# Kernel optimization log

Hardware: AMD Instinct MI355X
Metric: run time of the kernel (lower is better)

Reference implementation:

```python
import jax, jax.numpy as jnp
import numpy as np
import math

MODEL_DIM = 256
NUM_HEADS = 8
HEAD_DIM = MODEL_DIM // NUM_HEADS
DEMAND_DIM = 3
H, W = 128, 256
N_COLLAB = 4


def conv1x1(x, w, b):
    # x: [B, Cin, H, W], w: [Cout, Cin], b: [Cout]
    return jnp.einsum('oi,bihw->bohw', w, x) + b[None, :, None, None]


def setup_inputs() -> dict:
    key = jax.random.key(0)
    ks = jax.random.split(key, 16)
    s = 0.02
    hid = MODEL_DIM // 2
    inp = {
        'ego_features': jax.random.normal(ks[0], (1, MODEL_DIM, H, W), jnp.float32),
        'ego_demand': jax.random.uniform(ks[1], (1, DEMAND_DIM, H, W), jnp.float32),
        'collaborator_features': jax.random.normal(ks[2], (N_COLLAB, MODEL_DIM, H, W), jnp.float32),
        'w_d1': jax.random.normal(ks[3], (hid, DEMAND_DIM), jnp.float32) * s,
        'b_d1': jnp.zeros((hid,), jnp.float32),
        'w_d2': jax.random.normal(ks[4], (MODEL_DIM, hid), jnp.float32) * s,
        'b_d2': jnp.zeros((MODEL_DIM,), jnp.float32),
        'wq': jax.random.normal(ks[5], (MODEL_DIM, MODEL_DIM), jnp.float32) * s,
        'bq': jnp.zeros((MODEL_DIM,), jnp.float32),
        'wk': jax.random.normal(ks[6], (MODEL_DIM, MODEL_DIM), jnp.float32) * s,
        'bk': jnp.zeros((MODEL_DIM,), jnp.float32),
        'wv': jax.random.normal(ks[7], (MODEL_DIM, MODEL_DIM), jnp.float32) * s,
        'bv': jnp.zeros((MODEL_DIM,), jnp.float32),
        'wo': jax.random.normal(ks[8], (MODEL_DIM, MODEL_DIM), jnp.float32) * s,
        'bo': jnp.zeros((MODEL_DIM,), jnp.float32),
        'pos_emb': jnp.zeros((1, MODEL_DIM, H, W), jnp.float32),
    }
    return inp


def reference(ego_features, ego_demand, collaborator_features,
              w_d1, b_d1, w_d2, b_d2, wq, bq, wk, bk, wv, bv, wo, bo, pos_emb):
    # demand encoder: 1x1 conv -> relu -> 1x1 conv
    enc = conv1x1(jax.nn.relu(conv1x1(ego_demand, w_d1, b_d1)), w_d2, b_d2)
    query_state = ego_features + enc + pos_emb  # [1, C, H, W]

    q = conv1x1(query_state, wq, bq).reshape(NUM_HEADS, HEAD_DIM, H, W)        # [M, d, H, W]
    k = conv1x1(collaborator_features, wk, bk).reshape(N_COLLAB, NUM_HEADS, HEAD_DIM, H, W)
    v = conv1x1(collaborator_features, wv, bv).reshape(N_COLLAB, NUM_HEADS, HEAD_DIM, H, W)

    scale = math.sqrt(HEAD_DIM)
    # per-pixel dot product over head_dim -> scores [N, M, H, W]
    scores = jnp.einsum('mdhw,nmdhw->nmhw', q, k) / scale
    attn = jax.nn.softmax(scores, axis=0)  # softmax over collaborators
    # weighted sum over collaborators -> [M, d, H, W]
    out = jnp.einsum('nmhw,nmdhw->mdhw', attn, v).reshape(1, MODEL_DIM, H, W)
    return conv1x1(out, wo, bo)  # [1, C, H, W]
```

## Files before the change

### kernel.cpp

```cpp
#include <hip/hip_runtime.h>
#include <stdint.h>

typedef __attribute__((ext_vector_type(8))) short short8;
typedef __attribute__((ext_vector_type(4))) float f32x4;

constexpr int C   = 256;
constexpr int HID = 128;
constexpr int P   = 32768;
constexpr int BN  = 64;
constexpr int XLD = 280;
constexpr int HLD = 136;
constexpr int RAWG = 1056;

constexpr unsigned OFF_WQ  = 0;
constexpr unsigned OFF_WK  = 65536;
constexpr unsigned OFF_WV  = 131072;
constexpr unsigned OFF_WO  = 196608;
constexpr unsigned OFF_WD2 = 262144;
constexpr unsigned W_TOTAL = 294912;

__device__ __forceinline__ unsigned f2b(float x) {
    unsigned u = __float_as_uint(x);
    return (u + 0x7FFFu + ((u >> 16) & 1u)) >> 16;
}
__device__ __forceinline__ float b2f(unsigned u) {
    return __uint_as_float(u << 16);
}

__global__ void cvt_weights(const float* __restrict__ wq, const float* __restrict__ wk,
                            const float* __restrict__ wv, const float* __restrict__ wo,
                            const float* __restrict__ wd2, unsigned short* __restrict__ dst) {
    unsigned i = blockIdx.x * 256 + threadIdx.x;
    if (i >= W_TOTAL) return;
    float v;
    if (i < OFF_WK)       v = wq[i];
    else if (i < OFF_WV)  v = wk[i - OFF_WK];
    else if (i < OFF_WO)  v = wv[i - OFF_WV];
    else if (i < OFF_WD2) v = wo[i - OFF_WO];
    else                  v = wd2[i - OFF_WD2];
    dst[i] = (unsigned short)f2b(v);
}

template <int K, int LD, int MI>
__device__ __forceinline__ void gemmW(const unsigned short* __restrict__ W,
                                      const unsigned short (&B)[BN][LD],
                                      int row0, int a, int q, f32x4 (*acc)[4]) {
#pragma unroll 2
    for (int ks = 0; ks < K / 32; ++ks) {
        const int kb = ks * 32 + q * 8;
        short8 af[MI], bf[4];
#pragma unroll
        for (int mi = 0; mi < MI; ++mi)
            af[mi] = *reinterpret_cast<const short8*>(W + (size_t)(row0 + mi * 16 + a) * K + kb);
#pragma unroll
        for (int ni = 0; ni < 4; ++ni)
            bf[ni] = *reinterpret_cast<const short8*>(&B[ni * 16 + a][kb]);
#pragma unroll
        for (int mi = 0; mi < MI; ++mi)
#pragma unroll
            for (int ni = 0; ni < 4; ++ni)
                acc[mi][ni] = __builtin_amdgcn_mfma_f32_16x16x32_bf16(af[mi], bf[ni], acc[mi][ni], 0, 0, 0);
    }
}

__device__ __forceinline__ void stage_ego(const float* __restrict__ s0,
                                          const float* __restrict__ s1,
                                          int t, int pix0, unsigned short (&X)[BN][XLD]) {
    const int cg = t >> 4;
    const int pb = 4 * (t & 15);
#pragma unroll
    for (int k = 0; k < 4; ++k) {
        const int c = 2 * cg + 64 * k;
        float4 ra = *reinterpret_cast<const float4*>(s0 + (size_t)c * P + pix0 + pb);
        float4 rb = *reinterpret_cast<const float4*>(s0 + (size_t)(c + 1) * P + pix0 + pb);
        float4 ta = *reinterpret_cast<const float4*>(s1 + (size_t)c * P + pix0 + pb);
        float4 tb = *reinterpret_cast<const float4*>(s1 + (size_t)(c + 1) * P + pix0 + pb);
        ra.x += ta.x; ra.y += ta.y; ra.z += ta.z; ra.w += ta.w;
        rb.x += tb.x; rb.y += tb.y; rb.z += tb.z; rb.w += tb.w;
        const float va[4] = {ra.x, ra.y, ra.z, ra.w};
        const float vb[4] = {rb.x, rb.y, rb.z, rb.w};
#pragma unroll
        for (int pi = 0; pi < 4; ++pi) {
            unsigned pk = f2b(va[pi]) | (f2b(vb[pi]) << 16);
            *reinterpret_cast<unsigned*>(&X[pb + pi][c]) = pk;
        }
    }
}

__device__ __forceinline__ void issue_col_tile(const float* __restrict__ src, int pix0,
                                               int w, int l, unsigned char* rawb) {
#pragma unroll
    for (int j = 0; j < 8; ++j) {
        const int g = w * 8 + j;
        const float* gp = src + (size_t)(4 * g + (l >> 4)) * P + pix0 + (l & 15) * 4;
        __builtin_amdgcn_global_load_lds(
            (const __attribute__((address_space(1))) void*)(uintptr_t)gp,
            (__attribute__((address_space(3))) void*)(unsigned)(uintptr_t)(rawb + g * RAWG),
            16, 0, 0);
    }
}

__device__ __forceinline__ void convert_raw(int t, const unsigned char* rawb,
                                            unsigned short (&X)[BN][XLD]) {
    const int cg = t >> 4;
    const int pb = 4 * (t & 15);
#pragma unroll
    for (int k = 0; k < 4; ++k) {
        const int c = 2 * cg + 64 * k;
        const unsigned base = (unsigned)(c >> 2) * RAWG + (unsigned)(c & 3) * 256 + (unsigned)pb * 4;
        float4 ra = *reinterpret_cast<const float4*>(rawb + base);
        float4 rb = *reinterpret_cast<const float4*>(rawb + base + 256);
        const float va[4] = {ra.x, ra.y, ra.z, ra.w};
        const float vb[4] = {rb.x, rb.y, rb.z, rb.w};
#pragma unroll
        for (int pi = 0; pi < 4; ++pi) {
            unsigned pk = f2b(va[pi]) | (f2b(vb[pi]) << 16);
            *reinterpret_cast<unsigned*>(&X[pb + pi][c]) = pk;
        }
    }
}

__global__ __launch_bounds__(512, 1) void dca_mfma(
    const float* __restrict__ ego, const float* __restrict__ dem,
    const float* __restrict__ col,
    const float* __restrict__ w_d1, const float* __restrict__ b_d1,
    const float* __restrict__ b_d2, const float* __restrict__ bq,
    const float* __restrict__ bk, const float* __restrict__ bv,
    const float* __restrict__ bo, const float* __restrict__ pos,
    const unsigned short* __restrict__ wbf, float* __restrict__ out)
{
    __shared__ __align__(16) unsigned short xT[BN][XLD];
    __shared__ __align__(16) unsigned char rawb[64 * RAWG];

    using H1T_t = unsigned short[BN][HLD];
    H1T_t& h1T = *reinterpret_cast<H1T_t*>(rawb);

    const int t = threadIdx.x;
    const int w = t >> 6;
    const int l = t & 63;
    const int a = l & 15;
    const int q = l >> 4;
    const int row0 = w * 32;
    const int pix0 = blockIdx.x * BN;

    stage_ego(ego, pos, t, pix0, xT);

    {
        const int hid0 = 2 * l;
        const float w10 = w_d1[hid0 * 3 + 0], w11 = w_d1[hid0 * 3 + 1], w12 = w_d1[hid0 * 3 + 2];
        const float w20 = w_d1[hid0 * 3 + 3], w21 = w_d1[hid0 * 3 + 4], w22 = w_d1[hid0 * 3 + 5];
        const float bb0 = b_d1[hid0], bb1 = b_d1[hid0 + 1];
#pragma unroll
        for (int k = 0; k < 8; ++k) {
            const int p = w + 8 * k;
            float d0 = dem[pix0 + p];
            float d1 = dem[P + pix0 + p];
            float d2v = dem[2 * P + pix0 + p];
            float h0 = fmaxf(bb0 + w10 * d0 + w11 * d1 + w12 * d2v, 0.0f);
            float h1v = fmaxf(bb1 + w20 * d0 + w21 * d1 + w22 * d2v, 0.0f);
            *reinterpret_cast<unsigned*>(&h1T[p][hid0]) = f2b(h0) | (f2b(h1v) << 16);
        }
    }
    __syncthreads();

    f32x4 vacc[2][4];

#pragma unroll
    for (int mi = 0; mi < 2; ++mi) {
        f32x4 bb = *reinterpret_cast<const f32x4*>(b_d2 + row0 + mi * 16 + q * 4);
#pragma unroll
        for (int ni = 0; ni < 4; ++ni) vacc[mi][ni] = bb;
    }
    gemmW<HID, HLD, 2>(wbf + OFF_WD2, h1T, row0, a, q, vacc);
#pragma unroll
    for (int mi = 0; mi < 2; ++mi) {
        const int cb = row0 + mi * 16 + q * 4;
#pragma unroll
        for (int ni = 0; ni < 4; ++ni) {
            unsigned* cell = reinterpret_cast<unsigned*>(&xT[ni * 16 + a][cb]);
            unsigned e0 = cell[0], e1 = cell[1];
            float o0 = vacc[mi][ni][0] + b2f(e0 & 0xFFFFu);
            float o1 = vacc[mi][ni][1] + b2f(e0 >> 16);
            float o2 = vacc[mi][ni][2] + b2f(e1 & 0xFFFFu);
            float o3 = vacc[mi][ni][3] + b2f(e1 >> 16);
            cell[0] = f2b(o0) | (f2b(o1) << 16);
            cell[1] = f2b(o2) | (f2b(o3) << 16);
        }
    }
    __syncthreads();

    issue_col_tile(col, pix0, w, l, rawb);

#pragma unroll
    for (int mi = 0; mi < 2; ++mi) {
        f32x4 bb = *reinterpret_cast<const f32x4*>(bq + row0 + mi * 16 + q * 4);
#pragma unroll
        for (int ni = 0; ni < 4; ++ni) vacc[mi][ni] = bb;
    }
    gemmW<C, XLD, 2>(wbf + OFF_WQ, xT, row0, a, q, vacc);
    unsigned qpk[2][4][2];
#pragma unroll
    for (int mi = 0; mi < 2; ++mi)
#pragma unroll
        for (int ni = 0; ni < 4; ++ni) {
            qpk[mi][ni][0] = f2b(vacc[mi][ni][0]) | (f2b(vacc[mi][ni][1]) << 16);
            qpk[mi][ni][1] = f2b(vacc[mi][ni][2]) | (f2b(vacc[mi][ni][3]) << 16);
        }

    float lrun[4];
#pragma unroll
    for (int ni = 0; ni < 4; ++ni) lrun[ni] = 0.0f;
    {
        const f32x4 z = {0.0f, 0.0f, 0.0f, 0.0f};
#pragma unroll
        for (int mi = 0; mi < 2; ++mi)
#pragma unroll
            for (int ni = 0; ni < 4; ++ni) vacc[mi][ni] = z;
    }
#pragma unroll 1
    for (int n = 0; n < 4; ++n) {
        __syncthreads();
        convert_raw(t, rawb, xT);
        __syncthreads();
        if (n < 3) issue_col_tile(col + (size_t)(n + 1) * C * P, pix0, w, l, rawb);
        float s[4];
#pragma unroll
        for (int ni = 0; ni < 4; ++ni) s[ni] = 0.0f;
#pragma unroll
        for (int mi = 0; mi < 2; ++mi) {
            f32x4 kacc[1][4];
            f32x4 bb = *reinterpret_cast<const f32x4*>(bk + row0 + mi * 16 + q * 4);
#pragma unroll
            for (int ni = 0; ni < 4; ++ni) kacc[0][ni] = bb;
            gemmW<C, XLD, 1>(wbf + OFF_WK, xT, row0 + mi * 16, a, q, kacc);
#pragma unroll
            for (int ni = 0; ni < 4; ++ni) {
                const unsigned u0 = qpk[mi][ni][0], u1 = qpk[mi][ni][1];
                float ps = s[ni];
                ps += b2f(u0 & 0xFFFFu) * kacc[0][ni][0];
                ps += b2f(u0 >> 16)     * kacc[0][ni][1];
                ps += b2f(u1 & 0xFFFFu) * kacc[0][ni][2];
                ps += b2f(u1 >> 16)     * kacc[0][ni][3];
                s[ni] = ps;
            }
        }
        float pp[4];
#pragma unroll
        for (int ni = 0; ni < 4; ++ni) {
            float ps = s[ni];
            ps += __shfl_xor(ps, 16);
            ps += __shfl_xor(ps, 32);
            pp[ni] = __expf(ps * 0.17677669529663687f);
            lrun[ni] += pp[ni];
        }
#pragma unroll
        for (int ni = 0; ni < 4; ++ni) {
            const float ip = 1.0f / pp[ni];
#pragma unroll
            for (int mi = 0; mi < 2; ++mi) vacc[mi][ni] *= ip;
        }
        gemmW<C, XLD, 2>(wbf + OFF_WV, xT, row0, a, q, vacc);
#pragma unroll
        for (int ni = 0; ni < 4; ++ni) {
#pragma unroll
            for (int mi = 0; mi < 2; ++mi) vacc[mi][ni] *= pp[ni];
        }
    }
#pragma unroll
    for (int ni = 0; ni < 4; ++ni) {
        float inv = 1.0f / lrun[ni];
#pragma unroll
        for (int mi = 0; mi < 2; ++mi) vacc[mi][ni] *= inv;
    }
#pragma unroll
    for (int mi = 0; mi < 2; ++mi) {
        f32x4 bb = *reinterpret_cast<const f32x4*>(bv + row0 + mi * 16 + q * 4);
#pragma unroll
        for (int ni = 0; ni < 4; ++ni) vacc[mi][ni] += bb;
    }

    __syncthreads();
#pragma unroll
    for (int mi = 0; mi < 2; ++mi) {
        const int cb = row0 + mi * 16 + q * 4;
#pragma unroll
        for (int ni = 0; ni < 4; ++ni) {
            unsigned* cell = reinterpret_cast<unsigned*>(&xT[ni * 16 + a][cb]);
            cell[0] = f2b(vacc[mi][ni][0]) | (f2b(vacc[mi][ni][1]) << 16);
            cell[1] = f2b(vacc[mi][ni][2]) | (f2b(vacc[mi][ni][3]) << 16);
        }
    }
    __syncthreads();
#pragma unroll
    for (int mi = 0; mi < 2; ++mi) {
        f32x4 bb = *reinterpret_cast<const f32x4*>(bo + row0 + mi * 16 + q * 4);
#pragma unroll
        for (int ni = 0; ni < 4; ++ni) vacc[mi][ni] = bb;
    }
    gemmW<C, XLD, 2>(wbf + OFF_WO, xT, row0, a, q, vacc);
#pragma unroll
    for (int mi = 0; mi < 2; ++mi) {
        const int cb = row0 + mi * 16 + q * 4;
#pragma unroll
        for (int ni = 0; ni < 4; ++ni) {
            const int pix = pix0 + ni * 16 + a;
#pragma unroll
            for (int r = 0; r < 4; ++r)
                out[(size_t)(cb + r) * P + pix] = vacc[mi][ni][r];
        }
    }
}

extern "C" void kernel_launch(void* const* d_in, const int* in_sizes, int n_in,
                              void* d_out, int out_size, void* d_ws, size_t ws_size,
                              hipStream_t stream) {
    const float* ego  = (const float*)d_in[0];
    const float* dem  = (const float*)d_in[1];
    const float* col  = (const float*)d_in[2];
    const float* w_d1 = (const float*)d_in[3];
    const float* b_d1 = (const float*)d_in[4];
    const float* w_d2 = (const float*)d_in[5];
    const float* b_d2 = (const float*)d_in[6];
    const float* wq   = (const float*)d_in[7];
    const float* bq   = (const float*)d_in[8];
    const float* wk   = (const float*)d_in[9];
    const float* bk   = (const float*)d_in[10];
    const float* wv   = (const float*)d_in[11];
    const float* bv   = (const float*)d_in[12];
    const float* wo   = (const float*)d_in[13];
    const float* bo   = (const float*)d_in[14];
    const float* pos  = (const float*)d_in[15];
    float* out = (float*)d_out;
    unsigned short* wbf = (unsigned short*)d_ws;

    hipLaunchKernelGGL(cvt_weights, dim3((W_TOTAL + 255) / 256), dim3(256), 0, stream,
                       wq, wk, wv, wo, w_d2, wbf);
    hipLaunchKernelGGL(dca_mfma, dim3(P / BN), dim3(512), 0, stream,
                       ego, dem, col, w_d1, b_d1, b_d2, bq, bk, bv, bo, pos, wbf, out);
}
```

Measured before the change: 349.6 us.

## Double-buffer collaborator tiles via register prefetch with XOR-swizzled LDS layout

Replaces the async global-to-LDS raw staging buffer and its separate convert pass with two bf16 tile buffers. Each collaborator's next tile is loaded into registers in halves and converted into the alternate buffer while the K/V GEMMs run on the current one. This removes one barrier pair per iteration and overlaps load latency with MFMA work. It also adds an XOR swizzle to the LDS column index to reduce bank conflicts, and raises launch bounds to two blocks per CU, which adds register pressure from the held float4 prefetch registers.

```diff
diff --git a/kernel.cpp b/kernel.cpp
--- a/kernel.cpp
+++ b/kernel.cpp
@@ -10,7 +10,6 @@
 constexpr int BN  = 64;
 constexpr int XLD = 280;
 constexpr int HLD = 136;
-constexpr int RAWG = 1056;
 
 constexpr unsigned OFF_WQ  = 0;
 constexpr unsigned OFF_WK  = 65536;
@@ -41,10 +40,11 @@
     dst[i] = (unsigned short)f2b(v);
 }
 
-template <int K, int LD, int MI>
+template <int K, int LD, int MI, bool SWZ>
 __device__ __forceinline__ void gemmW(const unsigned short* __restrict__ W,
-                                      const unsigned short (&B)[BN][LD],
+                                      const unsigned short* __restrict__ B,
                                       int row0, int a, int q, f32x4 (*acc)[4]) {
+    const int sw0 = (a >> 2) << 3;
 #pragma unroll 2
     for (int ks = 0; ks < K / 32; ++ks) {
         const int kb = ks * 32 + q * 8;
@@ -53,8 +53,10 @@
         for (int mi = 0; mi < MI; ++mi)
             af[mi] = *reinterpret_cast<const short8*>(W + (size_t)(row0 + mi * 16 + a) * K + kb);
 #pragma unroll
-        for (int ni = 0; ni < 4; ++ni)
-            bf[ni] = *reinterpret_cast<const short8*>(&B[ni * 16 + a][kb]);
+        for (int ni = 0; ni < 4; ++ni) {
+            const int col = SWZ ? (kb ^ sw0 ^ ((ni & 1) << 5)) : kb;
+            bf[ni] = *reinterpret_cast<const short8*>(B + (ni * 16 + a) * LD + col);
+        }
 #pragma unroll
         for (int mi = 0; mi < MI; ++mi)
 #pragma unroll
@@ -65,12 +67,14 @@
 
 __device__ __forceinline__ void stage_ego(const float* __restrict__ s0,
                                           const float* __restrict__ s1,
-                                          int t, int pix0, unsigned short (&X)[BN][XLD]) {
+                                          int t, int pix0, unsigned short* X) {
     const int cg = t >> 4;
     const int pb = 4 * (t & 15);
+    const int swz = (t & 7) << 3;
 #pragma unroll
     for (int k = 0; k < 4; ++k) {
         const int c = 2 * cg + 64 * k;
+        const int cs = c ^ swz;
         float4 ra = *reinterpret_cast<const float4*>(s0 + (size_t)c * P + pix0 + pb);
         float4 rb = *reinterpret_cast<const float4*>(s0 + (size_t)(c + 1) * P + pix0 + pb);
         float4 ta = *reinterpret_cast<const float4*>(s1 + (size_t)c * P + pix0 + pb);
@@ -82,45 +86,43 @@
 #pragma unroll
         for (int pi = 0; pi < 4; ++pi) {
             unsigned pk = f2b(va[pi]) | (f2b(vb[pi]) << 16);
-            *reinterpret_cast<unsigned*>(&X[pb + pi][c]) = pk;
-        }
-    }
-}
-
-__device__ __forceinline__ void issue_col_tile(const float* __restrict__ src, int pix0,
-                                               int w, int l, unsigned char* rawb) {
-#pragma unroll
-    for (int j = 0; j < 8; ++j) {
-        const int g = w * 8 + j;
-        const float* gp = src + (size_t)(4 * g + (l >> 4)) * P + pix0 + (l & 15) * 4;
-        __builtin_amdgcn_global_load_lds(
-            (const __attribute__((address_space(1))) void*)(uintptr_t)gp,
-            (__attribute__((address_space(3))) void*)(unsigned)(uintptr_t)(rawb + g * RAWG),
-            16, 0, 0);
-    }
-}
-
-__device__ __forceinline__ void convert_raw(int t, const unsigned char* rawb,
-                                            unsigned short (&X)[BN][XLD]) {
+            *reinterpret_cast<unsigned*>(X + (pb + pi) * XLD + cs) = pk;
+        }
+    }
+}
+
+__device__ __forceinline__ void issue_half(const float* __restrict__ src, int pix0,
+                                           int t, int k0, float4* s4) {
     const int cg = t >> 4;
     const int pb = 4 * (t & 15);
 #pragma unroll
-    for (int k = 0; k < 4; ++k) {
-        const int c = 2 * cg + 64 * k;
-        const unsigned base = (unsigned)(c >> 2) * RAWG + (unsigned)(c & 3) * 256 + (unsigned)pb * 4;
-        float4 ra = *reinterpret_cast<const float4*>(rawb + base);
-        float4 rb = *reinterpret_cast<const float4*>(rawb + base + 256);
+    for (int kk = 0; kk < 2; ++kk) {
+        const int c = 2 * cg + 64 * (k0 + kk);
+        s4[2 * kk]     = *reinterpret_cast<const float4*>(src + (size_t)c * P + pix0 + pb);
+        s4[2 * kk + 1] = *reinterpret_cast<const float4*>(src + (size_t)(c + 1) * P + pix0 + pb);
+    }
+}
+
+__device__ __forceinline__ void convert_half(unsigned short* X, int t, int k0,
+                                             const float4* s4) {
+    const int cg = t >> 4;
+    const int pb = 4 * (t & 15);
+    const int swz = (t & 7) << 3;
+#pragma unroll
+    for (int kk = 0; kk < 2; ++kk) {
+        const int cs = (2 * cg + 64 * (k0 + kk)) ^ swz;
+        const float4 ra = s4[2 * kk], rb = s4[2 * kk + 1];
         const float va[4] = {ra.x, ra.y, ra.z, ra.w};
         const float vb[4] = {rb.x, rb.y, rb.z, rb.w};
 #pragma unroll
         for (int pi = 0; pi < 4; ++pi) {
             unsigned pk = f2b(va[pi]) | (f2b(vb[pi]) << 16);
-            *reinterpret_cast<unsigned*>(&X[pb + pi][c]) = pk;
-        }
-    }
-}
-
-__global__ __launch_bounds__(512, 1) void dca_mfma(
+            *reinterpret_cast<unsigned*>(X + (pb + pi) * XLD + cs) = pk;
+        }
+    }
+}
+
+__global__ __launch_bounds__(512, 2) void dca_mfma(
     const float* __restrict__ ego, const float* __restrict__ dem,
     const float* __restrict__ col,
     const float* __restrict__ w_d1, const float* __restrict__ b_d1,
@@ -129,11 +131,9 @@
     const float* __restrict__ bo, const float* __restrict__ pos,
     const unsigned short* __restrict__ wbf, float* __restrict__ out)
 {
-    __shared__ __align__(16) unsigned short xT[BN][XLD];
-    __shared__ __align__(16) unsigned char rawb[64 * RAWG];
-
-    using H1T_t = unsigned short[BN][HLD];
-    H1T_t& h1T = *reinterpret_cast<H1T_t*>(rawb);
+    __shared__ __align__(16) unsigned short xbuf[2 * BN * XLD];
+    unsigned short* const x0 = xbuf;
+    unsigned short* const x1 = xbuf + BN * XLD;
 
     const int t = threadIdx.x;
     const int w = t >> 6;
@@ -143,7 +143,7 @@
     const int row0 = w * 32;
     const int pix0 = blockIdx.x * BN;
 
-    stage_ego(ego, pos, t, pix0, xT);
+    stage_ego(ego, pos, t, pix0, x0);
 
     {
         const int hid0 = 2 * l;
@@ -158,7 +158,7 @@
             float d2v = dem[2 * P + pix0 + p];
             float h0 = fmaxf(bb0 + w10 * d0 + w11 * d1 + w12 * d2v, 0.0f);
             float h1v = fmaxf(bb1 + w20 * d0 + w21 * d1 + w22 * d2v, 0.0f);
-            *reinterpret_cast<unsigned*>(&h1T[p][hid0]) = f2b(h0) | (f2b(h1v) << 16);
+            *reinterpret_cast<unsigned*>(x1 + p * HLD + hid0) = f2b(h0) | (f2b(h1v) << 16);
         }
     }
     __syncthreads();
@@ -171,13 +171,15 @@
 #pragma unroll
         for (int ni = 0; ni < 4; ++ni) vacc[mi][ni] = bb;
     }
-    gemmW<HID, HLD, 2>(wbf + OFF_WD2, h1T, row0, a, q, vacc);
+    gemmW<HID, HLD, 2, false>(wbf + OFF_WD2, x1, row0, a, q, vacc);
 #pragma unroll
     for (int mi = 0; mi < 2; ++mi) {
         const int cb = row0 + mi * 16 + q * 4;
 #pragma unroll
         for (int ni = 0; ni < 4; ++ni) {
-            unsigned* cell = reinterpret_cast<unsigned*>(&xT[ni * 16 + a][cb]);
+            const int row = ni * 16 + a;
+            const int cs = cb ^ ((a >> 2) << 3) ^ ((ni & 1) << 5);
+            unsigned* cell = reinterpret_cast<unsigned*>(x0 + row * XLD + cs);
             unsigned e0 = cell[0], e1 = cell[1];
             float o0 = vacc[mi][ni][0] + b2f(e0 & 0xFFFFu);
             float o1 = vacc[mi][ni][1] + b2f(e0 >> 16);
@@ -189,7 +191,8 @@
     }
     __syncthreads();
 
-    issue_col_tile(col, pix0, w, l, rawb);
+    float4 sA[4], sB[4];
+    issue_half(col, pix0, t, 0, sA);
 
 #pragma unroll
     for (int mi = 0; mi < 2; ++mi) {
@@ -197,7 +200,7 @@
 #pragma unroll
         for (int ni = 0; ni < 4; ++ni) vacc[mi][ni] = bb;
     }
-    gemmW<C, XLD, 2>(wbf + OFF_WQ, xT, row0, a, q, vacc);
+    gemmW<C, XLD, 2, true>(wbf + OFF_WQ, x0, row0, a, q, vacc);
     unsigned qpk[2][4][2];
 #pragma unroll
     for (int mi = 0; mi < 2; ++mi)
@@ -206,6 +209,12 @@
             qpk[mi][ni][0] = f2b(vacc[mi][ni][0]) | (f2b(vacc[mi][ni][1]) << 16);
             qpk[mi][ni][1] = f2b(vacc[mi][ni][2]) | (f2b(vacc[mi][ni][3]) << 16);
         }
+
+    convert_half(x1, t, 0, sA);
+    issue_half(col, pix0, t, 2, sB);
+    convert_half(x1, t, 2, sB);
+    issue_half(col + (size_t)C * P, pix0, t, 0, sA);
+    __syncthreads();
 
     float lrun[4];
 #pragma unroll
@@ -219,10 +228,8 @@
     }
 #pragma unroll 1
     for (int n = 0; n < 4; ++n) {
-        __syncthreads();
-        convert_raw(t, rawb, xT);
-        __syncthreads();
-        if (n < 3) issue_col_tile(col + (size_t)(n + 1) * C * P, pix0, w, l, rawb);
+        unsigned short* const rbuf = (n & 1) ? x0 : x1;
+        unsigned short* const wbuf = (n & 1) ? x1 : x0;
         float s[4];
 #pragma unroll
         for (int ni = 0; ni < 4; ++ni) s[ni] = 0.0f;
@@ -232,7 +239,7 @@
             f32x4 bb = *reinterpret_cast<const f32x4*>(bk + row0 + mi * 16 + q * 4);
 #pragma unroll
             for (int ni = 0; ni < 4; ++ni) kacc[0][ni] = bb;
-            gemmW<C, XLD, 1>(wbf + OFF_WK, xT, row0 + mi * 16, a, q, kacc);
+            gemmW<C, XLD, 1, true>(wbf + OFF_WK, rbuf, row0 + mi * 16, a, q, kacc);
 #pragma unroll
             for (int ni = 0; ni < 4; ++ni) {
                 const unsigned u0 = qpk[mi][ni][0], u1 = qpk[mi][ni][1];
@@ -244,6 +251,10 @@
                 s[ni] = ps;
             }
         }
+        if (n < 3) {
+            convert_half(wbuf, t, 0, sA);
+            issue_half(col + (size_t)(n + 1) * C * P, pix0, t, 2, sB);
+        }
         float pp[4];
 #pragma unroll
         for (int ni = 0; ni < 4; ++ni) {
@@ -259,12 +270,15 @@
 #pragma unroll
             for (int mi = 0; mi < 2; ++mi) vacc[mi][ni] *= ip;
         }
-        gemmW<C, XLD, 2>(wbf + OFF_WV, xT, row0, a, q, vacc);
+        gemmW<C, XLD, 2, true>(wbf + OFF_WV, rbuf, row0, a, q, vacc);
 #pragma unroll
         for (int ni = 0; ni < 4; ++ni) {
 #pragma unroll
             for (int mi = 0; mi < 2; ++mi) vacc[mi][ni] *= pp[ni];
         }
+        if (n < 3) convert_half(wbuf, t, 2, sB);
+        if (n < 2) issue_half(col + (size_t)(n + 2) * C * P, pix0, t, 0, sA);
+        __syncthreads();
     }
 #pragma unroll
     for (int ni = 0; ni < 4; ++ni) {
@@ -279,13 +293,14 @@
         for (int ni = 0; ni < 4; ++ni) vacc[mi][ni] += bb;
     }
 
-    __syncthreads();
 #pragma unroll
     for (int mi = 0; mi < 2; ++mi) {
         const int cb = row0 + mi * 16 + q * 4;
 #pragma unroll
         for (int ni = 0; ni < 4; ++ni) {
-            unsigned* cell = reinterpret_cast<unsigned*>(&xT[ni * 16 + a][cb]);
+            const int row = ni * 16 + a;
+            const int cs = cb ^ ((a >> 2) << 3) ^ ((ni & 1) << 5);
+            unsigned* cell = reinterpret_cast<unsigned*>(x0 + row * XLD + cs);
             cell[0] = f2b(vacc[mi][ni][0]) | (f2b(vacc[mi][ni][1]) << 16);
             cell[1] = f2b(vacc[mi][ni][2]) | (f2b(vacc[mi][ni][3]) << 16);
         }
@@ -297,7 +312,7 @@
 #pragma unroll
         for (int ni = 0; ni < 4; ++ni) vacc[mi][ni] = bb;
     }
-    gemmW<C, XLD, 2>(wbf + OFF_WO, xT, row0, a, q, vacc);
+    gemmW<C, XLD, 2, true>(wbf + OFF_WO, x0, row0, a, q, vacc);
 #pragma unroll
     for (int mi = 0; mi < 2; ++mi) {
         const int cb = row0 + mi * 16 + q * 4;
```

New measurement: 333.7 us. 1.05x faster.
